# Kernel optimization log

Measured on AMD Instinct MI355X. Metric: run time of the kernel, lower is better.

Reference implementation:

```python
import jax, jax.numpy as jnp
import numpy as np

N_NODES = 100000
N_RELS = 3
N_EDGES = 300000


def setup_inputs() -> dict:
    key = jax.random.key(0)
    ks = jax.random.split(key, 6)
    x = jax.random.normal(ks[0], (N_NODES, 128), dtype=jnp.float32)
    W1 = jax.random.normal(ks[1], (N_RELS, 128, 128), dtype=jnp.float32) * (128 ** -0.5)
    b1 = jnp.zeros((N_RELS, 128), dtype=jnp.float32)
    W2 = jax.random.normal(ks[2], (N_RELS, 128, 64), dtype=jnp.float32) * (128 ** -0.5)
    b2 = jnp.zeros((N_RELS, 64), dtype=jnp.float32)
    edges = jax.random.randint(ks[3], (N_RELS, 2, N_EDGES), 0, N_NODES, dtype=jnp.int64)
    return {"x": x, "W1": W1, "b1": b1, "W2": W2, "b2": b2, "edges": edges}


def _hetero_graphconv_layer(x, W, b, edges, n_nodes):
    """Sum over relations of GraphConv(norm='both'):
    y_r = D_in^{-1/2} A_r (D_out^{-1/2} x) W_r + b_r   (degrees clamped to >=1, DGL default).
    HeteroGraphConv default aggregate is 'sum'."""
    out = jnp.zeros((n_nodes, W.shape[-1]), dtype=x.dtype)
    ones = jnp.ones((edges.shape[-1],), dtype=x.dtype)
    for r in range(edges.shape[0]):  # small fixed loop over relation types
        src, dst = edges[r, 0], edges[r, 1]
        out_deg = jnp.clip(jax.ops.segment_sum(ones, src, num_segments=n_nodes), 1.0)
        in_deg = jnp.clip(jax.ops.segment_sum(ones, dst, num_segments=n_nodes), 1.0)
        # transform scaled source features, then sparse aggregate to destinations
        m = (x * (out_deg ** -0.5)[:, None]) @ W[r]          # [N, out_f]
        agg = jax.ops.segment_sum(m[src], dst, num_segments=n_nodes)  # SpMM via gather+scatter
        out = out + agg * (in_deg ** -0.5)[:, None] + b[r]
    return out


def reference(x, W1, b1, W2, b2, edges):
    n = x.shape[0]
    h = jax.nn.relu(_hetero_graphconv_layer(x, W1, b1, edges, n))
    h = jax.nn.relu(_hetero_graphconv_layer(h, W2, b2, edges, n))
    return h
```

## Files before the change

kernel.cpp:

```cpp
#include <hip/hip_runtime.h>
#include <hip/hip_bf16.h>
#include <stdint.h>


constexpr int TPB = 256;

typedef __attribute__((ext_vector_type(8))) short short8;
typedef __attribute__((ext_vector_type(4))) float f32x4;

__device__ __forceinline__ float bf2f(unsigned short u) {
    return __uint_as_float(((unsigned)u) << 16);
}
__device__ __forceinline__ unsigned short f2bf(float f) {
    return __bfloat16_as_ushort(__float2bfloat16(f));
}


__global__ void count_kernel(const int* __restrict__ edges, unsigned* __restrict__ cnt,
                             int total, int E, int N) {
    int i = blockIdx.x * blockDim.x + threadIdx.x;
    if (i >= total) return;
    atomicAdd(&cnt[(size_t)(i / E) * N + edges[i]], 1u);
}

__global__ __launch_bounds__(256) void scan_local_kernel(const unsigned* __restrict__ cnt,
                                                         int* __restrict__ off,
                                                         unsigned* __restrict__ bsum,
                                                         int N, int nb) {
    int r = blockIdx.x / nb, blk = blockIdx.x - r * nb;
    const unsigned* in = cnt + (size_t)(2 * r + 1) * N;
    int* o = off + (size_t)r * (N + 1);
    const int t = threadIdx.x, lane = t & 63, wid = t >> 6;
    int base = blk * 1024 + t * 4;
    unsigned v0 = (base + 0 < N) ? in[base + 0] : 0u;
    unsigned v1 = (base + 1 < N) ? in[base + 1] : 0u;
    unsigned v2 = (base + 2 < N) ? in[base + 2] : 0u;
    unsigned v3 = (base + 3 < N) ? in[base + 3] : 0u;
    unsigned p1 = v0, p2 = p1 + v1, p3 = p2 + v2, tt = p3 + v3;
    unsigned x = tt;
#pragma unroll
    for (int d = 1; d < 64; d <<= 1) {
        unsigned tmp = __shfl_up(x, d, 64);
        if (lane >= d) x += tmp;
    }
    __shared__ unsigned ws4[4];
    if (lane == 63) ws4[wid] = x;
    __syncthreads();
    unsigned woff = 0;
#pragma unroll
    for (int w2 = 0; w2 < 4; ++w2)
        if (w2 < wid) woff += ws4[w2];
    unsigned excl = woff + x - tt;
    if (base + 0 < N) o[base + 0] = (int)excl;
    if (base + 1 < N) o[base + 1] = (int)(excl + p1);
    if (base + 2 < N) o[base + 2] = (int)(excl + p2);
    if (base + 3 < N) o[base + 3] = (int)(excl + p3);
    if (t == 255) bsum[r * nb + blk] = woff + x;
}

__global__ __launch_bounds__(128) void scan_bsum_kernel(unsigned* __restrict__ bsum,
                                                        int* __restrict__ off,
                                                        int nb, int N, int E) {
    const int t = threadIdx.x, lane = t & 63, wid = t >> 6;
    __shared__ unsigned wtot[2];
    for (int r = 0; r < 3; ++r) {
        unsigned v = (t < nb) ? bsum[r * nb + t] : 0u;
        unsigned x = v;
#pragma unroll
        for (int d = 1; d < 64; d <<= 1) {
            unsigned tmp = __shfl_up(x, d, 64);
            if (lane >= d) x += tmp;
        }
        if (lane == 63) wtot[wid] = x;
        __syncthreads();
        unsigned add = (wid == 1) ? wtot[0] : 0u;
        if (t < nb) bsum[r * nb + t] = add + x - v;
        if (t == 0) off[(size_t)r * (N + 1) + N] = E;
        __syncthreads();
    }
}

__global__ void finalize_off_kernel(int* __restrict__ off, const unsigned* __restrict__ bsum,
                                    int* __restrict__ cur, int N, int nb) {
    int i = blockIdx.x * blockDim.x + threadIdx.x;
    if (i >= 3 * N) return;
    int r = i / N, n = i - r * N;
    int v = off[(size_t)r * (N + 1) + n] + (int)bsum[r * nb + (n >> 10)];
    off[(size_t)r * (N + 1) + n] = v;
    cur[i] = v;
}

__global__ void fill_kernel(const int* __restrict__ edges, int* __restrict__ cur,
                            int* __restrict__ csr_src, int E, int N) {
    int gid = blockIdx.x * blockDim.x + threadIdx.x;
    if (gid >= 3 * E) return;
    int r = gid / E, e = gid - r * E;
    int d  = edges[(size_t)(2 * r + 1) * E + e];
    int sv = edges[(size_t)(2 * r) * E + e];
    int pos = atomicAdd(&cur[(size_t)r * N + d], 1);
    csr_src[(size_t)r * E + pos] = sv;
}

__global__ void scale_inplace_kernel(unsigned* __restrict__ buf, int total) {
    int i = blockIdx.x * blockDim.x + threadIdx.x;
    if (i >= total) return;
    unsigned c = buf[i];
    ((float*)buf)[i] = rsqrtf((float)(c ? c : 1u));
}


template <int CH, typename XT>
__global__ __launch_bounds__(256) void mfma_gemm3_kernel(const XT* __restrict__ X,
                                                         const float* __restrict__ W,
                                                         int WS, int c0,
                                                         const float* __restrict__ s,
                                                         __hip_bfloat16* __restrict__ T, int N) {
    constexpr int CT = CH / 16;
    constexpr int FR = 4 * CT;
    __shared__ short bs[3 * FR * 512];
    const int t = threadIdx.x;
    const int lane = t & 63, wv = t >> 6;
    const int m0 = blockIdx.x * 64;

    constexpr int TOT = 3 * 32 * CH;
    for (int linear = t; linear < TOT; linear += 256) {
        int rrel = linear / (32 * CH);
        int rem = linear - rrel * (32 * CH);
        int r4 = rem / CH, cc = rem - r4 * CH;
        int r = r4 << 2;
        const float* wp = W + (size_t)rrel * 128 * WS + (size_t)r * WS + c0 + cc;
        unsigned u0 = f2bf(wp[0]);
        unsigned u1 = f2bf(wp[WS]);
        unsigned u2 = f2bf(wp[2 * WS]);
        unsigned u3 = f2bf(wp[3 * WS]);
        int kk = r4 >> 3, jg = (r4 >> 1) & 3, j0 = (r4 & 1) * 4;
        int l = jg * 16 + (cc & 15), c = cc >> 4;
        int slot = ((rrel * FR + kk * CT + c) << 9) + l * 8 + j0;
        *reinterpret_cast<uint2*>(&bs[slot]) = make_uint2(u0 | (u1 << 16), u2 | (u3 << 16));
    }

    const int row = m0 + wv * 16 + (lane & 15);
    const bool ok = row < N;
    short8 a[4];
    if constexpr (sizeof(XT) == 4) {
        const float* xr = (const float*)X + (size_t)row * 128 + ((lane >> 4) << 3);
#pragma unroll
        for (int kk = 0; kk < 4; ++kk) {
            short8 av = {};
            if (ok) {
                float4 f0 = *reinterpret_cast<const float4*>(xr + kk * 32);
                float4 f1 = *reinterpret_cast<const float4*>(xr + kk * 32 + 4);
                av[0] = (short)f2bf(f0.x); av[1] = (short)f2bf(f0.y);
                av[2] = (short)f2bf(f0.z); av[3] = (short)f2bf(f0.w);
                av[4] = (short)f2bf(f1.x); av[5] = (short)f2bf(f1.y);
                av[6] = (short)f2bf(f1.z); av[7] = (short)f2bf(f1.w);
            }
            a[kk] = av;
        }
    } else {
        const short* xr = (const short*)X + (size_t)row * 128 + ((lane >> 4) << 3);
#pragma unroll
        for (int kk = 0; kk < 4; ++kk) {
            short8 av = {};
            if (ok) av = *reinterpret_cast<const short8*>(xr + kk * 32);
            a[kk] = av;
        }
    }

    __syncthreads();

    f32x4 acc4[3 * CT];
#pragma unroll
    for (int f = 0; f < 3 * CT; ++f) acc4[f] = {0.f, 0.f, 0.f, 0.f};
#pragma unroll
    for (int rrel = 0; rrel < 3; ++rrel) {
#pragma unroll
        for (int c = 0; c < CT; ++c) {
#pragma unroll
            for (int kk = 0; kk < 4; ++kk) {
                short8 b = *reinterpret_cast<const short8*>(
                    &bs[((rrel * FR + kk * CT + c) << 9) + lane * 8]);
                acc4[rrel * CT + c] =
                    __builtin_amdgcn_mfma_f32_16x16x32_bf16(a[kk], b, acc4[rrel * CT + c], 0, 0, 0);
            }
        }
    }

#pragma unroll
    for (int rrel = 0; rrel < 3; ++rrel) {
        const float* so = s + (size_t)(2 * rrel) * N;
        __hip_bfloat16* Tr = T + (size_t)rrel * N * CH;
#pragma unroll
        for (int q = 0; q < 4; ++q) {
            int grow = m0 + wv * 16 + ((lane >> 4) << 2) + q;
            if (grow < N) {
                float sc = so[grow];
#pragma unroll
                for (int c = 0; c < CT; ++c) {
                    int gcol = c * 16 + (lane & 15);
                    Tr[(size_t)grow * CH + gcol] = __float2bfloat16(acc4[rrel * CT + c][q] * sc);
                }
            }
        }
    }
}


template <int CH, int PHASE>
__global__ __launch_bounds__(256) void gather3_kernel(const int* __restrict__ off,
                                                      const int* __restrict__ csr,
                                                      const __hip_bfloat16* __restrict__ T,
                                                      const float* __restrict__ s,
                                                      const float* __restrict__ b, int FT, int c0,
                                                      float* __restrict__ outp,
                                                      __hip_bfloat16* __restrict__ h,
                                                      int N, int E) {
    int gid = blockIdx.x * blockDim.x + threadIdx.x;
    int n = gid >> 3;
    if (n >= N) return;
    int j = (gid & 7) << 3;
    int bj = c0 + j;
    float o[8];
#pragma unroll
    for (int k = 0; k < 8; ++k)
        o[k] = b[bj + k] + b[FT + bj + k] + b[2 * FT + bj + k];
#pragma unroll
    for (int r = 0; r < 3; ++r) {
        const int* offr = off + (size_t)r * (N + 1);
        const int* csrr = csr + (size_t)r * E;
        const __hip_bfloat16* Tr = T + (size_t)r * N * CH;
        int e0 = offr[n], e1 = offr[n + 1];
        float acc[8];
#pragma unroll
        for (int k = 0; k < 8; ++k) acc[k] = 0.f;
        int e = e0;
        for (; e + 2 <= e1; e += 2) {
            int p0 = csrr[e], p1 = csrr[e + 1];
            short8 r0 = *reinterpret_cast<const short8*>(&Tr[(size_t)p0 * CH + j]);
            short8 r1 = *reinterpret_cast<const short8*>(&Tr[(size_t)p1 * CH + j]);
#pragma unroll
            for (int k = 0; k < 8; ++k)
                acc[k] += bf2f((unsigned short)r0[k]) + bf2f((unsigned short)r1[k]);
        }
        if (e < e1) {
            int p0 = csrr[e];
            short8 r0 = *reinterpret_cast<const short8*>(&Tr[(size_t)p0 * CH + j]);
#pragma unroll
            for (int k = 0; k < 8; ++k) acc[k] += bf2f((unsigned short)r0[k]);
        }
        float si = s[(size_t)(2 * r + 1) * N + n];
#pragma unroll
        for (int k = 0; k < 8; ++k) o[k] += si * acc[k];
    }
    if constexpr (PHASE == 0) {
        short8 pk;
#pragma unroll
        for (int k = 0; k < 8; ++k) pk[k] = (short)f2bf(fmaxf(o[k], 0.f));
        *reinterpret_cast<short8*>(&h[(size_t)n * 128 + c0 + j]) = pk;
    } else {
        float4 v0, v1;
        v0.x = fmaxf(o[0], 0.f); v0.y = fmaxf(o[1], 0.f);
        v0.z = fmaxf(o[2], 0.f); v0.w = fmaxf(o[3], 0.f);
        v1.x = fmaxf(o[4], 0.f); v1.y = fmaxf(o[5], 0.f);
        v1.z = fmaxf(o[6], 0.f); v1.w = fmaxf(o[7], 0.f);
        float* p = &outp[(size_t)n * 64 + j];
        *reinterpret_cast<float4*>(p) = v0;
        *reinterpret_cast<float4*>(p + 4) = v1;
    }
}

static inline int cdiv(int a, int b) { return (a + b - 1) / b; }

extern "C" void kernel_launch(void* const* d_in, const int* in_sizes, int n_in,
                              void* d_out, int out_size, void* d_ws, size_t ws_size,
                              hipStream_t stream) {
    const float* x  = (const float*)d_in[0];
    const float* W1 = (const float*)d_in[1];
    const float* b1 = (const float*)d_in[2];
    const float* W2 = (const float*)d_in[3];
    const float* b2 = (const float*)d_in[4];
    const int*   edges = (const int*)d_in[5];
    float* out = (float*)d_out;

    const int N = in_sizes[0] / 128;
    const int E = in_sizes[5] / 6;
    const int nb = cdiv(N, 1024);
    constexpr int CH = 64;

    auto align256 = [](char* p) { return (char*)(((uintptr_t)p + 255) & ~(uintptr_t)255); };
    char* w = (char*)d_ws;
    unsigned* cnt = (unsigned*)w;
    float* s = (float*)w;                       w = align256(w + (size_t)6 * N * 4);
    __hip_bfloat16* T = (__hip_bfloat16*)w;     w = align256(w + (size_t)3 * N * CH * 2);
    int* off = (int*)w;                         w = align256(w + (size_t)3 * (N + 1) * 4);
    int* csr = (int*)w;
    int* cur = (int*)T;
    unsigned* bsum = (unsigned*)((char*)T + (size_t)3 * N * 4 + 256);
    __hip_bfloat16* h = (__hip_bfloat16*)d_out;

    hipMemsetAsync(cnt, 0, (size_t)6 * N * 4, stream);
    count_kernel<<<cdiv(6 * E, TPB), TPB, 0, stream>>>(edges, cnt, 6 * E, E, N);
    scan_local_kernel<<<3 * nb, 256, 0, stream>>>(cnt, off, bsum, N, nb);
    scan_bsum_kernel<<<1, 128, 0, stream>>>(bsum, off, nb, N, E);
    finalize_off_kernel<<<cdiv(3 * N, TPB), TPB, 0, stream>>>(off, bsum, cur, N, nb);
    fill_kernel<<<cdiv(3 * E, TPB), TPB, 0, stream>>>(edges, cur, csr, E, N);
    scale_inplace_kernel<<<cdiv(6 * N, TPB), TPB, 0, stream>>>(cnt, 6 * N);

    const int mgrid = cdiv(N, 64);
    const int ggrid = cdiv(N * 8, TPB);

    for (int c0 = 0; c0 < 128; c0 += CH) {
        mfma_gemm3_kernel<CH, float><<<mgrid, 256, 0, stream>>>(x, W1, 128, c0, s, T, N);
        gather3_kernel<CH, 0><<<ggrid, TPB, 0, stream>>>(off, csr, T, s, b1, 128, c0,
                                                         nullptr, h, N, E);
    }
    mfma_gemm3_kernel<CH, __hip_bfloat16><<<mgrid, 256, 0, stream>>>(h, W2, 64, 0, s, T, N);
    gather3_kernel<CH, 1><<<ggrid, TPB, 0, stream>>>(off, csr, T, s, b2, 64, 0,
                                                     out, nullptr, N, E);
}
```

Before: 461.2 us.

## Merge per-relation CSRs into one unified CSR with relation-tagged sources

Builds a single destination-indexed CSR over all three relations, packing the relation id into the high bits of each source index. The gather kernel then walks one edge list per node with a 4-way unrolled loop, picking the per-relation in-degree scale by tag, in place of three separate short loops. The scan and finalize kernels shrink to one relation's worth of offsets. This cuts per-relation offset loads and loop overhead and exposes more independent loads per thread. In exchange it adds per-edge select logic and assumes node ids fit in 17 bits.

```diff
diff --git a/kernel.cpp b/kernel.cpp
--- a/kernel.cpp
+++ b/kernel.cpp
@@ -26,17 +26,18 @@
 __global__ __launch_bounds__(256) void scan_local_kernel(const unsigned* __restrict__ cnt,
                                                          int* __restrict__ off,
                                                          unsigned* __restrict__ bsum,
-                                                         int N, int nb) {
-    int r = blockIdx.x / nb, blk = blockIdx.x - r * nb;
-    const unsigned* in = cnt + (size_t)(2 * r + 1) * N;
-    int* o = off + (size_t)r * (N + 1);
+                                                         int N) {
+    int blk = blockIdx.x;
     const int t = threadIdx.x, lane = t & 63, wid = t >> 6;
     int base = blk * 1024 + t * 4;
-    unsigned v0 = (base + 0 < N) ? in[base + 0] : 0u;
-    unsigned v1 = (base + 1 < N) ? in[base + 1] : 0u;
-    unsigned v2 = (base + 2 < N) ? in[base + 2] : 0u;
-    unsigned v3 = (base + 3 < N) ? in[base + 3] : 0u;
-    unsigned p1 = v0, p2 = p1 + v1, p3 = p2 + v2, tt = p3 + v3;
+    unsigned v[4];
+#pragma unroll
+    for (int k = 0; k < 4; ++k) {
+        int i = base + k;
+        v[k] = (i < N) ? (cnt[(size_t)N + i] + cnt[(size_t)3 * N + i] + cnt[(size_t)5 * N + i])
+                       : 0u;
+    }
+    unsigned p1 = v[0], p2 = p1 + v[1], p3 = p2 + v[2], tt = p3 + v[3];
     unsigned x = tt;
 #pragma unroll
     for (int d = 1; d < 64; d <<= 1) {
@@ -51,54 +52,50 @@
     for (int w2 = 0; w2 < 4; ++w2)
         if (w2 < wid) woff += ws4[w2];
     unsigned excl = woff + x - tt;
-    if (base + 0 < N) o[base + 0] = (int)excl;
-    if (base + 1 < N) o[base + 1] = (int)(excl + p1);
-    if (base + 2 < N) o[base + 2] = (int)(excl + p2);
-    if (base + 3 < N) o[base + 3] = (int)(excl + p3);
-    if (t == 255) bsum[r * nb + blk] = woff + x;
+    if (base + 0 < N) off[base + 0] = (int)excl;
+    if (base + 1 < N) off[base + 1] = (int)(excl + p1);
+    if (base + 2 < N) off[base + 2] = (int)(excl + p2);
+    if (base + 3 < N) off[base + 3] = (int)(excl + p3);
+    if (t == 255) bsum[blk] = woff + x;
 }
 
 __global__ __launch_bounds__(128) void scan_bsum_kernel(unsigned* __restrict__ bsum,
                                                         int* __restrict__ off,
-                                                        int nb, int N, int E) {
+                                                        int nb, int N, int TE) {
     const int t = threadIdx.x, lane = t & 63, wid = t >> 6;
     __shared__ unsigned wtot[2];
-    for (int r = 0; r < 3; ++r) {
-        unsigned v = (t < nb) ? bsum[r * nb + t] : 0u;
-        unsigned x = v;
-#pragma unroll
-        for (int d = 1; d < 64; d <<= 1) {
-            unsigned tmp = __shfl_up(x, d, 64);
-            if (lane >= d) x += tmp;
-        }
-        if (lane == 63) wtot[wid] = x;
-        __syncthreads();
-        unsigned add = (wid == 1) ? wtot[0] : 0u;
-        if (t < nb) bsum[r * nb + t] = add + x - v;
-        if (t == 0) off[(size_t)r * (N + 1) + N] = E;
-        __syncthreads();
-    }
+    unsigned v = (t < nb) ? bsum[t] : 0u;
+    unsigned x = v;
+#pragma unroll
+    for (int d = 1; d < 64; d <<= 1) {
+        unsigned tmp = __shfl_up(x, d, 64);
+        if (lane >= d) x += tmp;
+    }
+    if (lane == 63) wtot[wid] = x;
+    __syncthreads();
+    unsigned add = (wid == 1) ? wtot[0] : 0u;
+    if (t < nb) bsum[t] = add + x - v;
+    if (t == 0) off[N] = TE;
 }
 
 __global__ void finalize_off_kernel(int* __restrict__ off, const unsigned* __restrict__ bsum,
-                                    int* __restrict__ cur, int N, int nb) {
+                                    int* __restrict__ cur, int N) {
     int i = blockIdx.x * blockDim.x + threadIdx.x;
-    if (i >= 3 * N) return;
-    int r = i / N, n = i - r * N;
-    int v = off[(size_t)r * (N + 1) + n] + (int)bsum[r * nb + (n >> 10)];
-    off[(size_t)r * (N + 1) + n] = v;
+    if (i >= N) return;
+    int v = off[i] + (int)bsum[i >> 10];
+    off[i] = v;
     cur[i] = v;
 }
 
 __global__ void fill_kernel(const int* __restrict__ edges, int* __restrict__ cur,
-                            int* __restrict__ csr_src, int E, int N) {
+                            int* __restrict__ csr, int E, int N) {
     int gid = blockIdx.x * blockDim.x + threadIdx.x;
     if (gid >= 3 * E) return;
     int r = gid / E, e = gid - r * E;
     int d  = edges[(size_t)(2 * r + 1) * E + e];
     int sv = edges[(size_t)(2 * r) * E + e];
-    int pos = atomicAdd(&cur[(size_t)r * N + d], 1);
-    csr_src[(size_t)r * E + pos] = sv;
+    int pos = atomicAdd(&cur[d], 1);
+    csr[pos] = (r << 17) | sv;
 }
 
 __global__ void scale_inplace_kernel(unsigned* __restrict__ buf, int total) {
@@ -207,14 +204,14 @@
 
 
 template <int CH, int PHASE>
-__global__ __launch_bounds__(256) void gather3_kernel(const int* __restrict__ off,
-                                                      const int* __restrict__ csr,
-                                                      const __hip_bfloat16* __restrict__ T,
-                                                      const float* __restrict__ s,
-                                                      const float* __restrict__ b, int FT, int c0,
-                                                      float* __restrict__ outp,
-                                                      __hip_bfloat16* __restrict__ h,
-                                                      int N, int E) {
+__global__ __launch_bounds__(256) void gather_u_kernel(const int* __restrict__ off,
+                                                       const int* __restrict__ csr,
+                                                       const __hip_bfloat16* __restrict__ T,
+                                                       const float* __restrict__ s,
+                                                       const float* __restrict__ b, int FT, int c0,
+                                                       float* __restrict__ outp,
+                                                       __hip_bfloat16* __restrict__ h,
+                                                       int N) {
     int gid = blockIdx.x * blockDim.x + threadIdx.x;
     int n = gid >> 3;
     if (n >= N) return;
@@ -224,34 +221,47 @@
 #pragma unroll
     for (int k = 0; k < 8; ++k)
         o[k] = b[bj + k] + b[FT + bj + k] + b[2 * FT + bj + k];
-#pragma unroll
-    for (int r = 0; r < 3; ++r) {
-        const int* offr = off + (size_t)r * (N + 1);
-        const int* csrr = csr + (size_t)r * E;
-        const __hip_bfloat16* Tr = T + (size_t)r * N * CH;
-        int e0 = offr[n], e1 = offr[n + 1];
-        float acc[8];
-#pragma unroll
-        for (int k = 0; k < 8; ++k) acc[k] = 0.f;
-        int e = e0;
-        for (; e + 2 <= e1; e += 2) {
-            int p0 = csrr[e], p1 = csrr[e + 1];
-            short8 r0 = *reinterpret_cast<const short8*>(&Tr[(size_t)p0 * CH + j]);
-            short8 r1 = *reinterpret_cast<const short8*>(&Tr[(size_t)p1 * CH + j]);
-#pragma unroll
-            for (int k = 0; k < 8; ++k)
-                acc[k] += bf2f((unsigned short)r0[k]) + bf2f((unsigned short)r1[k]);
-        }
-        if (e < e1) {
-            int p0 = csrr[e];
-            short8 r0 = *reinterpret_cast<const short8*>(&Tr[(size_t)p0 * CH + j]);
-#pragma unroll
-            for (int k = 0; k < 8; ++k) acc[k] += bf2f((unsigned short)r0[k]);
-        }
-        float si = s[(size_t)(2 * r + 1) * N + n];
-#pragma unroll
-        for (int k = 0; k < 8; ++k) o[k] += si * acc[k];
-    }
+
+    const float si0 = s[(size_t)1 * N + n];
+    const float si1 = s[(size_t)3 * N + n];
+    const float si2 = s[(size_t)5 * N + n];
+
+    int e0 = off[n], e1 = off[n + 1];
+    int e = e0;
+    for (; e + 4 <= e1; e += 4) {
+        int v0 = csr[e], v1 = csr[e + 1], v2 = csr[e + 2], v3 = csr[e + 3];
+        int r0 = v0 >> 17, r1 = v1 >> 17, r2 = v2 >> 17, r3 = v3 >> 17;
+        const short8* p0 = reinterpret_cast<const short8*>(
+            &T[((size_t)r0 * N + (v0 & 0x1FFFF)) * CH + j]);
+        const short8* p1 = reinterpret_cast<const short8*>(
+            &T[((size_t)r1 * N + (v1 & 0x1FFFF)) * CH + j]);
+        const short8* p2 = reinterpret_cast<const short8*>(
+            &T[((size_t)r2 * N + (v2 & 0x1FFFF)) * CH + j]);
+        const short8* p3 = reinterpret_cast<const short8*>(
+            &T[((size_t)r3 * N + (v3 & 0x1FFFF)) * CH + j]);
+        short8 t0 = *p0, t1 = *p1, t2 = *p2, t3 = *p3;
+        float w0 = r0 == 0 ? si0 : (r0 == 1 ? si1 : si2);
+        float w1 = r1 == 0 ? si0 : (r1 == 1 ? si1 : si2);
+        float w2 = r2 == 0 ? si0 : (r2 == 1 ? si1 : si2);
+        float w3 = r3 == 0 ? si0 : (r3 == 1 ? si1 : si2);
+#pragma unroll
+        for (int k = 0; k < 8; ++k) {
+            o[k] += w0 * bf2f((unsigned short)t0[k]);
+            o[k] += w1 * bf2f((unsigned short)t1[k]);
+            o[k] += w2 * bf2f((unsigned short)t2[k]);
+            o[k] += w3 * bf2f((unsigned short)t3[k]);
+        }
+    }
+    for (; e < e1; ++e) {
+        int v0 = csr[e];
+        int r0 = v0 >> 17;
+        short8 t0 = *reinterpret_cast<const short8*>(
+            &T[((size_t)r0 * N + (v0 & 0x1FFFF)) * CH + j]);
+        float w0 = r0 == 0 ? si0 : (r0 == 1 ? si1 : si2);
+#pragma unroll
+        for (int k = 0; k < 8; ++k) o[k] += w0 * bf2f((unsigned short)t0[k]);
+    }
+
     if constexpr (PHASE == 0) {
         short8 pk;
 #pragma unroll
@@ -292,17 +302,17 @@
     unsigned* cnt = (unsigned*)w;
     float* s = (float*)w;                       w = align256(w + (size_t)6 * N * 4);
     __hip_bfloat16* T = (__hip_bfloat16*)w;     w = align256(w + (size_t)3 * N * CH * 2);
-    int* off = (int*)w;                         w = align256(w + (size_t)3 * (N + 1) * 4);
+    int* off = (int*)w;                         w = align256(w + (size_t)(N + 1) * 4);
     int* csr = (int*)w;
     int* cur = (int*)T;
-    unsigned* bsum = (unsigned*)((char*)T + (size_t)3 * N * 4 + 256);
+    unsigned* bsum = (unsigned*)((char*)T + (size_t)N * 4 + 256);
     __hip_bfloat16* h = (__hip_bfloat16*)d_out;
 
     hipMemsetAsync(cnt, 0, (size_t)6 * N * 4, stream);
     count_kernel<<<cdiv(6 * E, TPB), TPB, 0, stream>>>(edges, cnt, 6 * E, E, N);
-    scan_local_kernel<<<3 * nb, 256, 0, stream>>>(cnt, off, bsum, N, nb);
-    scan_bsum_kernel<<<1, 128, 0, stream>>>(bsum, off, nb, N, E);
-    finalize_off_kernel<<<cdiv(3 * N, TPB), TPB, 0, stream>>>(off, bsum, cur, N, nb);
+    scan_local_kernel<<<nb, 256, 0, stream>>>(cnt, off, bsum, N);
+    scan_bsum_kernel<<<1, 128, 0, stream>>>(bsum, off, nb, N, 3 * E);
+    finalize_off_kernel<<<cdiv(N, TPB), TPB, 0, stream>>>(off, bsum, cur, N);
     fill_kernel<<<cdiv(3 * E, TPB), TPB, 0, stream>>>(edges, cur, csr, E, N);
     scale_inplace_kernel<<<cdiv(6 * N, TPB), TPB, 0, stream>>>(cnt, 6 * N);
 
@@ -311,10 +321,10 @@
 
     for (int c0 = 0; c0 < 128; c0 += CH) {
         mfma_gemm3_kernel<CH, float><<<mgrid, 256, 0, stream>>>(x, W1, 128, c0, s, T, N);
-        gather3_kernel<CH, 0><<<ggrid, TPB, 0, stream>>>(off, csr, T, s, b1, 128, c0,
-                                                         nullptr, h, N, E);
+        gather_u_kernel<CH, 0><<<ggrid, TPB, 0, stream>>>(off, csr, T, s, b1, 128, c0,
+                                                          nullptr, h, N);
     }
     mfma_gemm3_kernel<CH, __hip_bfloat16><<<mgrid, 256, 0, stream>>>(h, W2, 64, 0, s, T, N);
-    gather3_kernel<CH, 1><<<ggrid, TPB, 0, stream>>>(off, csr, T, s, b2, 64, 0,
-                                                     out, nullptr, N, E);
-}
+    gather_u_kernel<CH, 1><<<ggrid, TPB, 0, stream>>>(off, csr, T, s, b2, 64, 0,
+                                                      out, nullptr, N);
+}
```

After: 440.0 us. 1.05x faster.
